# Kernel optimization log

Measured on AMD Instinct MI355X. Metric: run time of the kernel, lower is better.

The kernel has to match this reference:

```python
import jax, jax.numpy as jnp
import numpy as np

VAR_EPS = 1e-05


def setup_inputs() -> dict:
    key = jax.random.key(0)
    k1, k2 = jax.random.split(key)
    B, T = 1024, 16384
    pred = jax.random.normal(k1, (B, T), dtype=jnp.float32)
    target = jax.random.normal(k2, (B, T), dtype=jnp.float32)
    return {"pred": pred, "target": target}


def reference(pred, target):
    # Per-row Pearson correlation, vectorized over the batch dimension.
    T = pred.shape[1]
    mp = jnp.mean(pred, axis=1, keepdims=True)
    mt = jnp.mean(target, axis=1, keepdims=True)
    cp = pred - mp                      # [B, T] centered
    ct = target - mt
    sp = jnp.sum(cp * cp, axis=1)       # [B] sum of squares
    st = jnp.sum(ct * ct, axis=1)
    num = jnp.sum(cp * ct, axis=1)      # [B] covariance numerator
    # torch.var uses unbiased estimator (correction=1)
    var_p = sp / (T - 1)
    var_t = st / (T - 1)
    denom = jnp.sqrt(sp * st)
    safe_denom = jnp.where(denom > 0, denom, 1.0)
    corr = num / safe_denom
    valid = (var_p > VAR_EPS) & (var_t > VAR_EPS) & (denom > 0) & ~jnp.isnan(corr)
    per_row = jnp.where(valid, 1.0 - corr, 1.0)
    return jnp.mean(per_row)
```

## Files before the change

kernel.cpp:

```cpp
#include <hip/hip_runtime.h>

#define T_LEN 16384
#define VAR_EPS 1e-5f

__global__ __launch_bounds__(512) void pearson_row_kernel(
    const float* __restrict__ pred, const float* __restrict__ target,
    float* __restrict__ out, float inv_B)
{
    const int row = blockIdx.x;
    const int tid = threadIdx.x;
    const float4* __restrict__ p4 =
        (const float4*)(pred + (size_t)row * T_LEN);
    const float4* __restrict__ t4 =
        (const float4*)(target + (size_t)row * T_LEN);

    float sp = 0.f, st = 0.f, spp = 0.f, stt = 0.f, spt = 0.f;

    #pragma unroll
    for (int half = 0; half < 2; ++half) {
        const int i0 = tid + half * 2048;
        float4 a0 = p4[i0];
        float4 a1 = p4[i0 + 512];
        float4 a2 = p4[i0 + 1024];
        float4 a3 = p4[i0 + 1536];
        float4 b0 = t4[i0];
        float4 b1 = t4[i0 + 512];
        float4 b2 = t4[i0 + 1024];
        float4 b3 = t4[i0 + 1536];

        sp  += (a0.x + a0.y + a0.z + a0.w) + (a1.x + a1.y + a1.z + a1.w)
             + (a2.x + a2.y + a2.z + a2.w) + (a3.x + a3.y + a3.z + a3.w);
        st  += (b0.x + b0.y + b0.z + b0.w) + (b1.x + b1.y + b1.z + b1.w)
             + (b2.x + b2.y + b2.z + b2.w) + (b3.x + b3.y + b3.z + b3.w);
        spp += a0.x*a0.x + a0.y*a0.y + a0.z*a0.z + a0.w*a0.w
             + a1.x*a1.x + a1.y*a1.y + a1.z*a1.z + a1.w*a1.w
             + a2.x*a2.x + a2.y*a2.y + a2.z*a2.z + a2.w*a2.w
             + a3.x*a3.x + a3.y*a3.y + a3.z*a3.z + a3.w*a3.w;
        stt += b0.x*b0.x + b0.y*b0.y + b0.z*b0.z + b0.w*b0.w
             + b1.x*b1.x + b1.y*b1.y + b1.z*b1.z + b1.w*b1.w
             + b2.x*b2.x + b2.y*b2.y + b2.z*b2.z + b2.w*b2.w
             + b3.x*b3.x + b3.y*b3.y + b3.z*b3.z + b3.w*b3.w;
        spt += a0.x*b0.x + a0.y*b0.y + a0.z*b0.z + a0.w*b0.w
             + a1.x*b1.x + a1.y*b1.y + a1.z*b1.z + a1.w*b1.w
             + a2.x*b2.x + a2.y*b2.y + a2.z*b2.z + a2.w*b2.w
             + a3.x*b3.x + a3.y*b3.y + a3.z*b3.z + a3.w*b3.w;
    }

    #pragma unroll
    for (int off = 32; off > 0; off >>= 1) {
        sp  += __shfl_down(sp,  off);
        st  += __shfl_down(st,  off);
        spp += __shfl_down(spp, off);
        stt += __shfl_down(stt, off);
        spt += __shfl_down(spt, off);
    }

    __shared__ float ws[8][5];
    const int lane = tid & 63;
    const int wave = tid >> 6;
    if (lane == 0) {
        ws[wave][0] = sp;  ws[wave][1] = st;  ws[wave][2] = spp;
        ws[wave][3] = stt; ws[wave][4] = spt;
    }
    __syncthreads();

    if (tid == 0) {
        float S_p = 0.f, S_t = 0.f, S_pp = 0.f, S_tt = 0.f, S_pt = 0.f;
        #pragma unroll
        for (int w = 0; w < 8; ++w) {
            S_p  += ws[w][0]; S_t  += ws[w][1]; S_pp += ws[w][2];
            S_tt += ws[w][3]; S_pt += ws[w][4];
        }

        const float T   = (float)T_LEN;
        const float inv = 1.0f / T;
        float cp2 = S_pp - S_p * S_p * inv;
        float ct2 = S_tt - S_t * S_t * inv;
        float num = S_pt - S_p * S_t * inv;

        float var_p = cp2 / (T - 1.0f);
        float var_t = ct2 / (T - 1.0f);
        float denom = sqrtf(cp2 * ct2);
        float safe  = (denom > 0.0f) ? denom : 1.0f;
        float corr  = num / safe;
        bool valid = (var_p > VAR_EPS) && (var_t > VAR_EPS) &&
                     (denom > 0.0f) && !isnan(corr);
        float loss = valid ? (1.0f - corr) : 1.0f;
        atomicAdd(out, loss * inv_B);
    }
}

extern "C" void kernel_launch(void* const* d_in, const int* in_sizes, int n_in,
                              void* d_out, int out_size, void* d_ws, size_t ws_size,
                              hipStream_t stream) {
    const float* pred   = (const float*)d_in[0];
    const float* target = (const float*)d_in[1];
    float* out = (float*)d_out;

    const int B = in_sizes[0] / T_LEN;

    hipMemsetAsync(out, 0, sizeof(float), stream);
    pearson_row_kernel<<<B, 512, 0, stream>>>(pred, target, out, 1.0f / (float)B);
}
```

Baseline: 144.9 us.

## Split each row across four blocks with atomic moments and a final reduction kernel

```diff
diff --git a/kernel.cpp b/kernel.cpp
--- a/kernel.cpp
+++ b/kernel.cpp
@@ -1,50 +1,48 @@
 #include <hip/hip_runtime.h>
 
 #define T_LEN 16384
+#define Q4    1024
 #define VAR_EPS 1e-5f
 
-__global__ __launch_bounds__(512) void pearson_row_kernel(
+__global__ __launch_bounds__(256) void pearson_partial_kernel(
     const float* __restrict__ pred, const float* __restrict__ target,
-    float* __restrict__ out, float inv_B)
+    float* __restrict__ moments)
 {
-    const int row = blockIdx.x;
+    const int blk = blockIdx.x;
+    const int row = blk >> 2;
+    const int q   = blk & 3;
     const int tid = threadIdx.x;
+
     const float4* __restrict__ p4 =
-        (const float4*)(pred + (size_t)row * T_LEN);
+        (const float4*)(pred + (size_t)row * T_LEN) + q * Q4;
     const float4* __restrict__ t4 =
-        (const float4*)(target + (size_t)row * T_LEN);
+        (const float4*)(target + (size_t)row * T_LEN) + q * Q4;
 
-    float sp = 0.f, st = 0.f, spp = 0.f, stt = 0.f, spt = 0.f;
+    float4 a0 = p4[tid];
+    float4 a1 = p4[tid + 256];
+    float4 a2 = p4[tid + 512];
+    float4 a3 = p4[tid + 768];
+    float4 b0 = t4[tid];
+    float4 b1 = t4[tid + 256];
+    float4 b2 = t4[tid + 512];
+    float4 b3 = t4[tid + 768];
 
-    #pragma unroll
-    for (int half = 0; half < 2; ++half) {
-        const int i0 = tid + half * 2048;
-        float4 a0 = p4[i0];
-        float4 a1 = p4[i0 + 512];
-        float4 a2 = p4[i0 + 1024];
-        float4 a3 = p4[i0 + 1536];
-        float4 b0 = t4[i0];
-        float4 b1 = t4[i0 + 512];
-        float4 b2 = t4[i0 + 1024];
-        float4 b3 = t4[i0 + 1536];
-
-        sp  += (a0.x + a0.y + a0.z + a0.w) + (a1.x + a1.y + a1.z + a1.w)
-             + (a2.x + a2.y + a2.z + a2.w) + (a3.x + a3.y + a3.z + a3.w);
-        st  += (b0.x + b0.y + b0.z + b0.w) + (b1.x + b1.y + b1.z + b1.w)
-             + (b2.x + b2.y + b2.z + b2.w) + (b3.x + b3.y + b3.z + b3.w);
-        spp += a0.x*a0.x + a0.y*a0.y + a0.z*a0.z + a0.w*a0.w
-             + a1.x*a1.x + a1.y*a1.y + a1.z*a1.z + a1.w*a1.w
-             + a2.x*a2.x + a2.y*a2.y + a2.z*a2.z + a2.w*a2.w
-             + a3.x*a3.x + a3.y*a3.y + a3.z*a3.z + a3.w*a3.w;
-        stt += b0.x*b0.x + b0.y*b0.y + b0.z*b0.z + b0.w*b0.w
-             + b1.x*b1.x + b1.y*b1.y + b1.z*b1.z + b1.w*b1.w
-             + b2.x*b2.x + b2.y*b2.y + b2.z*b2.z + b2.w*b2.w
-             + b3.x*b3.x + b3.y*b3.y + b3.z*b3.z + b3.w*b3.w;
-        spt += a0.x*b0.x + a0.y*b0.y + a0.z*b0.z + a0.w*b0.w
-             + a1.x*b1.x + a1.y*b1.y + a1.z*b1.z + a1.w*b1.w
-             + a2.x*b2.x + a2.y*b2.y + a2.z*b2.z + a2.w*b2.w
-             + a3.x*b3.x + a3.y*b3.y + a3.z*b3.z + a3.w*b3.w;
-    }
+    float sp  = (a0.x + a0.y + a0.z + a0.w) + (a1.x + a1.y + a1.z + a1.w)
+              + (a2.x + a2.y + a2.z + a2.w) + (a3.x + a3.y + a3.z + a3.w);
+    float st  = (b0.x + b0.y + b0.z + b0.w) + (b1.x + b1.y + b1.z + b1.w)
+              + (b2.x + b2.y + b2.z + b2.w) + (b3.x + b3.y + b3.z + b3.w);
+    float spp = a0.x*a0.x + a0.y*a0.y + a0.z*a0.z + a0.w*a0.w
+              + a1.x*a1.x + a1.y*a1.y + a1.z*a1.z + a1.w*a1.w
+              + a2.x*a2.x + a2.y*a2.y + a2.z*a2.z + a2.w*a2.w
+              + a3.x*a3.x + a3.y*a3.y + a3.z*a3.z + a3.w*a3.w;
+    float stt = b0.x*b0.x + b0.y*b0.y + b0.z*b0.z + b0.w*b0.w
+              + b1.x*b1.x + b1.y*b1.y + b1.z*b1.z + b1.w*b1.w
+              + b2.x*b2.x + b2.y*b2.y + b2.z*b2.z + b2.w*b2.w
+              + b3.x*b3.x + b3.y*b3.y + b3.z*b3.z + b3.w*b3.w;
+    float spt = a0.x*b0.x + a0.y*b0.y + a0.z*b0.z + a0.w*b0.w
+              + a1.x*b1.x + a1.y*b1.y + a1.z*b1.z + a1.w*b1.w
+              + a2.x*b2.x + a2.y*b2.y + a2.z*b2.z + a2.w*b2.w
+              + a3.x*b3.x + a3.y*b3.y + a3.z*b3.z + a3.w*b3.w;
 
     #pragma unroll
     for (int off = 32; off > 0; off >>= 1) {
@@ -55,22 +53,29 @@
         spt += __shfl_down(spt, off);
     }
 
-    __shared__ float ws[8][5];
-    const int lane = tid & 63;
-    const int wave = tid >> 6;
-    if (lane == 0) {
-        ws[wave][0] = sp;  ws[wave][1] = st;  ws[wave][2] = spp;
-        ws[wave][3] = stt; ws[wave][4] = spt;
+    if ((tid & 63) == 0) {
+        float* m = moments + row * 8;
+        atomicAdd(m + 0, sp);
+        atomicAdd(m + 1, st);
+        atomicAdd(m + 2, spp);
+        atomicAdd(m + 3, stt);
+        atomicAdd(m + 4, spt);
     }
-    __syncthreads();
+}
 
-    if (tid == 0) {
-        float S_p = 0.f, S_t = 0.f, S_pp = 0.f, S_tt = 0.f, S_pt = 0.f;
-        #pragma unroll
-        for (int w = 0; w < 8; ++w) {
-            S_p  += ws[w][0]; S_t  += ws[w][1]; S_pp += ws[w][2];
-            S_tt += ws[w][3]; S_pt += ws[w][4];
-        }
+__global__ __launch_bounds__(1024) void pearson_final_kernel(
+    const float* __restrict__ moments, float* __restrict__ out, int B)
+{
+    const int tid = threadIdx.x;
+    float loss_sum = 0.f;
+
+    for (int r = tid; r < B; r += 1024) {
+        const float* m = moments + r * 8;
+        float S_p  = m[0];
+        float S_t  = m[1];
+        float S_pp = m[2];
+        float S_tt = m[3];
+        float S_pt = m[4];
 
         const float T   = (float)T_LEN;
         const float inv = 1.0f / T;
@@ -85,8 +90,22 @@
         float corr  = num / safe;
         bool valid = (var_p > VAR_EPS) && (var_t > VAR_EPS) &&
                      (denom > 0.0f) && !isnan(corr);
-        float loss = valid ? (1.0f - corr) : 1.0f;
-        atomicAdd(out, loss * inv_B);
+        loss_sum += valid ? (1.0f - corr) : 1.0f;
+    }
+
+    #pragma unroll
+    for (int off = 32; off > 0; off >>= 1)
+        loss_sum += __shfl_down(loss_sum, off);
+
+    __shared__ float ws[16];
+    if ((tid & 63) == 0) ws[tid >> 6] = loss_sum;
+    __syncthreads();
+
+    if (tid == 0) {
+        float tot = 0.f;
+        #pragma unroll
+        for (int w = 0; w < 16; ++w) tot += ws[w];
+        out[0] = tot / (float)B;
     }
 }
 
@@ -95,10 +114,12 @@
                               hipStream_t stream) {
     const float* pred   = (const float*)d_in[0];
     const float* target = (const float*)d_in[1];
-    float* out = (float*)d_out;
+    float* out     = (float*)d_out;
+    float* moments = (float*)d_ws;
 
     const int B = in_sizes[0] / T_LEN;
 
-    hipMemsetAsync(out, 0, sizeof(float), stream);
-    pearson_row_kernel<<<B, 512, 0, stream>>>(pred, target, out, 1.0f / (float)B);
+    hipMemsetAsync(moments, 0, (size_t)B * 8 * sizeof(float), stream);
+    pearson_partial_kernel<<<B * 4, 256, 0, stream>>>(pred, target, moments);
+    pearson_final_kernel<<<1, 1024, 0, stream>>>(moments, out, B);
 }
```

Result: no change. 144.0 us (-0.6%).
